# Kernel optimization log

Measured on AMD Instinct MI355X. Metric: run time of the kernel, lower is better.

Reference implementation:

```python
import jax, jax.numpy as jnp
import numpy as np

N_NODES = 20000
N_EDGES = 160000
N_GRAPHS = 64
DIMS = [9, 128, 256, 512, 1534]
NEG_SLOPE_ATT = 0.2   # GATConv attention LeakyReLU
NEG_SLOPE_ACT = 0.01  # nn.LeakyReLU between layers
EPS = 1e-5            # GraphNorm eps


def setup_inputs() -> dict:
    key = jax.random.key(0)
    inp = {}
    k, key = jax.random.split(key)
    inp['x'] = jax.random.normal(k, (N_NODES, DIMS[0]), jnp.float32)
    k, key = jax.random.split(key)
    inp['edge_index'] = jax.random.randint(k, (2, N_EDGES), 0, N_NODES)
    k, key = jax.random.split(key)
    inp['batch'] = jnp.sort(jax.random.randint(k, (N_NODES,), 0, N_GRAPHS))
    for l in range(4):
        din, dout = DIMS[l], DIMS[l + 1]
        k1, k2, k3, key = jax.random.split(key, 4)
        s = 1.0 / np.sqrt(din)
        inp[f'W{l}'] = (jax.random.normal(k1, (din, dout)) * s).astype(jnp.float32)
        inp[f'asrc{l}'] = (jax.random.normal(k2, (dout,)) * 0.1).astype(jnp.float32)
        inp[f'adst{l}'] = (jax.random.normal(k3, (dout,)) * 0.1).astype(jnp.float32)
        inp[f'b{l}'] = jnp.zeros((dout,), jnp.float32)
        inp[f'g{l}'] = jnp.ones((dout,), jnp.float32)   # GraphNorm weight
        inp[f'bt{l}'] = jnp.zeros((dout,), jnp.float32)  # GraphNorm bias
        inp[f'ms{l}'] = jnp.ones((dout,), jnp.float32)   # GraphNorm mean_scale
    return inp


def _gat_conv(h, src, dst, n, W, asrc, adst, b):
    # PyG GATConv, heads=1: linear (no bias), edge attention, segment softmax, scatter-add
    hp = h @ W                                                    # [N, dout]
    e = jax.nn.leaky_relu((hp @ asrc)[src] + (hp @ adst)[dst], NEG_SLOPE_ATT)  # [E]
    m = jax.ops.segment_max(e, dst, num_segments=n)
    m = jnp.where(jnp.isfinite(m), m, 0.0)
    ex = jnp.exp(e - m[dst])
    denom = jax.ops.segment_sum(ex, dst, num_segments=n)
    alpha = ex / (denom[dst] + 1e-16)                             # [E]
    out = jax.ops.segment_sum(alpha[:, None] * hp[src], dst, num_segments=n)
    return out + b


def _graph_norm(h, batch, counts, g, bt, ms):
    # PyG GraphNorm: per-graph mean/var with learnable mean_scale
    mean = jax.ops.segment_sum(h, batch, num_segments=N_GRAPHS) / counts
    out = h - ms * mean[batch]
    var = jax.ops.segment_sum(out * out, batch, num_segments=N_GRAPHS) / counts
    return out / jnp.sqrt(var[batch] + EPS) * g + bt


def _forward(x, edge_index, batch, params):
    n = x.shape[0]
    loops = jnp.arange(n)
    src = jnp.concatenate([edge_index[0], loops])   # GATConv add_self_loops=True
    dst = jnp.concatenate([edge_index[1], loops])
    counts = jax.ops.segment_sum(jnp.ones((n,), x.dtype), batch, num_segments=N_GRAPHS)[:, None]
    h = x
    for (W, asrc, adst, b, g, bt, ms) in params:
        h = _gat_conv(h, src, dst, n, W, asrc, adst, b)
        h = jax.nn.leaky_relu(h, NEG_SLOPE_ACT)
        h = _graph_norm(h, batch, counts, g, bt, ms)
        # Dropout(p=0.1) is identity in eval mode
    mean = (jax.ops.segment_sum(h, batch, num_segments=N_GRAPHS) / counts)[:, None, :]
    mx = jax.ops.segment_max(h, batch, num_segments=N_GRAPHS)[:, None, :]
    return jnp.concatenate([mean, mx], axis=1)      # [G, 2, 1534]


def reference(x, edge_index, batch,
              W0, asrc0, adst0, b0, g0, bt0, ms0,
              W1, asrc1, adst1, b1, g1, bt1, ms1,
              W2, asrc2, adst2, b2, g2, bt2, ms2,
              W3, asrc3, adst3, b3, g3, bt3, ms3):
    params = [
        (W0, asrc0, adst0, b0, g0, bt0, ms0),
        (W1, asrc1, adst1, b1, g1, bt1, ms1),
        (W2, asrc2, adst2, b2, g2, bt2, ms2),
        (W3, asrc3, adst3, b3, g3, bt3, ms3),
    ]
    return _forward(x, edge_index, batch, params)
```

## Files before the change

### kernel.cpp

```cpp
#include <hip/hip_runtime.h>
#include <math.h>

typedef unsigned int u32;
typedef unsigned short u16;
using half8 = __attribute__((ext_vector_type(8))) _Float16;
using f32x4 = __attribute__((ext_vector_type(4))) float;

#define NN 20000
#define MPAD 20096
#define NE 160000
#define ET 180000
#define NG 64
#define NBLK 79

constexpr float NEG_ATT = 0.2f;
constexpr float NEG_ACT = 0.01f;
constexpr float EPS_GN  = 1e-5f;

struct Ptr4 { const float *p0, *p1, *p2, *p3; };


__device__ __forceinline__ u16 f2h(float f) {
    _Float16 h = (_Float16)f;
    return __builtin_bit_cast(u16, h);
}
__device__ __forceinline__ float h2f(u16 b) {
    return (float)__builtin_bit_cast(_Float16, b);
}

__device__ __forceinline__ void gl_lds16(const void* g, void* l) {
    __builtin_amdgcn_global_load_lds((const __attribute__((address_space(1))) u32*)g,
                                     (__attribute__((address_space(3))) u32*)l, 16, 0, 0);
}

__device__ __forceinline__ float lrelu_att(float v) {
    return (v > 0.f) ? v : NEG_ATT * v;
}


__global__ void k_bounds(const int* __restrict__ batch, int* __restrict__ counts,
                         int* __restrict__ gstart) {
    __shared__ int ls[NG + 1];
    int g = threadIdx.x;
    int lo = 0, hi = NN;
    while (lo < hi) {
        int mid = (lo + hi) >> 1;
        if (batch[mid] < g) lo = mid + 1; else hi = mid;
    }
    ls[g] = lo;
    if (g == 0) ls[NG] = NN;
    __syncthreads();
    counts[g] = ls[g + 1] - ls[g];
    gstart[g] = ls[g];
    if (g == 0) gstart[NG] = NN;
}


__global__ void k_deg(const int* __restrict__ ei, int* deg) {
    int i = blockIdx.x * 256 + threadIdx.x;
    if (i >= ET) return;
    int dst = (i < NE) ? ei[NE + i] : (i - NE);
    atomicAdd(&deg[dst], 1);
}

__global__ void k_scan1(const int* __restrict__ deg, int* __restrict__ bsum) {
    int i = blockIdx.x * 256 + threadIdx.x;
    int v = (i < NN) ? deg[i] : 0;
    int lane = threadIdx.x & 63, w = threadIdx.x >> 6;
    #pragma unroll
    for (int off = 32; off; off >>= 1) v += __shfl_down(v, off, 64);
    __shared__ int ws[4];
    if (lane == 0) ws[w] = v;
    __syncthreads();
    if (threadIdx.x == 0) bsum[blockIdx.x] = ws[0] + ws[1] + ws[2] + ws[3];
}

__global__ void k_scan2(const int* __restrict__ bsum, int* __restrict__ boff,
                        int* __restrict__ total) {
    int tid = threadIdx.x;
    int v = (tid < NBLK) ? bsum[tid] : 0;
    int lane = tid & 63, w = tid >> 6;
    int val = v;
    #pragma unroll
    for (int off = 1; off < 64; off <<= 1) {
        int t = __shfl_up(val, off, 64);
        if (lane >= off) val += t;
    }
    __shared__ int ws[4];
    if (lane == 63) ws[w] = val;
    __syncthreads();
    int woff = 0;
    for (int k = 0; k < w; k++) woff += ws[k];
    int excl = woff + val - v;
    if (tid < NBLK) boff[tid] = excl;
    if (tid == NBLK - 1) *total = excl + v;
}

__global__ void k_scan3(const int* __restrict__ deg, const int* __restrict__ boff,
                        int* __restrict__ row_ptr, int* __restrict__ cursor) {
    int i = blockIdx.x * 256 + threadIdx.x;
    int v = (i < NN) ? deg[i] : 0;
    int lane = threadIdx.x & 63, w = threadIdx.x >> 6;
    int val = v;
    #pragma unroll
    for (int off = 1; off < 64; off <<= 1) {
        int t = __shfl_up(val, off, 64);
        if (lane >= off) val += t;
    }
    __shared__ int ws[4];
    if (lane == 63) ws[w] = val;
    __syncthreads();
    int woff = 0;
    for (int k = 0; k < w; k++) woff += ws[k];
    int excl = boff[blockIdx.x] + woff + val - v;
    if (i < NN) { row_ptr[i] = excl; cursor[i] = excl; }
}

__global__ void k_scatter(const int* __restrict__ ei, int* cursor, int* __restrict__ col) {
    int i = blockIdx.x * 256 + threadIdx.x;
    if (i >= ET) return;
    int s, d;
    if (i < NE) { s = ei[i]; d = ei[NE + i]; } else { s = i - NE; d = s; }
    int p = atomicAdd(&cursor[d], 1);
    col[p] = s;
}


__global__ void k_wvec_all(Ptr4 W, Ptr4 As, Ptr4 Ad,
                           float* __restrict__ wsrcA, float* __restrict__ wdstA) {
    const int dins[4]  = {9, 128, 256, 512};
    const int douts[4] = {128, 256, 512, 1534};
    int l = blockIdx.y, k = blockIdx.x;
    if (k >= dins[l]) return;
    const float* Wp = (l == 0) ? W.p0 : (l == 1) ? W.p1 : (l == 2) ? W.p2 : W.p3;
    const float* as = (l == 0) ? As.p0 : (l == 1) ? As.p1 : (l == 2) ? As.p2 : As.p3;
    const float* ad = (l == 0) ? Ad.p0 : (l == 1) ? Ad.p1 : (l == 2) ? Ad.p2 : Ad.p3;
    int NC = douts[l];
    const float* row = Wp + (size_t)k * NC;
    float ss = 0.f, sd = 0.f;
    for (int n = threadIdx.x; n < NC; n += 256) {
        float w = row[n];
        ss += w * as[n];
        sd += w * ad[n];
    }
    __shared__ float ls[8];
    int lane = threadIdx.x & 63, w4 = threadIdx.x >> 6;
    #pragma unroll
    for (int off = 32; off; off >>= 1) {
        ss += __shfl_down(ss, off, 64);
        sd += __shfl_down(sd, off, 64);
    }
    if (lane == 0) { ls[w4] = ss; ls[4 + w4] = sd; }
    __syncthreads();
    if (threadIdx.x == 0) {
        wsrcA[l * 512 + k] = ls[0] + ls[1] + ls[2] + ls[3];
        wdstA[l * 512 + k] = ls[4] + ls[5] + ls[6] + ls[7];
    }
}


__global__ void k_wbt_all(Ptr4 W, u16* __restrict__ WbTall) {
    const int Ks[3] = {128, 256, 512};
    const int NCs[3] = {256, 512, 1534};
    const int Nps[3] = {256, 512, 1536};
    const size_t offs[3] = {0, 256 * 128, 256 * 128 + 512 * 256};
    int l = blockIdx.z;
    int K = Ks[l], NC = NCs[l], Np = Nps[l];
    int n0 = blockIdx.x * 32, k0 = blockIdx.y * 32;
    if (n0 >= Np || k0 >= K) return;
    const float* Wp = (l == 0) ? W.p1 : (l == 1) ? W.p2 : W.p3;
    u16* WbT = WbTall + offs[l];
    __shared__ u16 tile[32][33];
    int tx = threadIdx.x & 31, ty = threadIdx.x >> 5;
    #pragma unroll
    for (int i = 0; i < 4; i++) {
        int k = k0 + ty + i * 8, n = n0 + tx;
        float v = (k < K && n < NC) ? Wp[(size_t)k * NC + n] : 0.f;
        tile[ty + i * 8][tx] = f2h(v);
    }
    __syncthreads();
    #pragma unroll
    for (int i = 0; i < 4; i++) {
        int n = n0 + ty + i * 8, k = k0 + tx;
        if (n < Np && k < K) WbT[(size_t)n * K + k] = tile[tx][ty + i * 8];
    }
}


__global__ void k_scores0(const float* __restrict__ x, const float* __restrict__ wsrc,
                          const float* __restrict__ wdst, float* __restrict__ s_src,
                          float* __restrict__ s_dst) {
    int v = blockIdx.x * 256 + threadIdx.x;
    if (v >= NN) return;
    const float* r = x + (size_t)v * 9;
    float ss = 0.f, sd = 0.f;
    #pragma unroll
    for (int k = 0; k < 9; k++) { ss += r[k] * wsrc[k]; sd += r[k] * wdst[k]; }
    s_src[v] = ss; s_dst[v] = sd;
}

template <int VW>
__global__ void k_scores_h(const u16* __restrict__ h, const float* __restrict__ wsrc,
                           const float* __restrict__ wdst, float* __restrict__ s_src,
                           float* __restrict__ s_dst, int din) {
    int v = blockIdx.x * 4 + (threadIdx.x >> 6);
    int lane = threadIdx.x & 63;
    if (v >= NN) return;
    const u16* row = h + (size_t)v * din;
    float ss = 0.f, sd = 0.f;
    for (int d = lane * VW; d < din; d += 64 * VW) {
        u32 ua[VW / 2];
        if constexpr (VW == 2) {
            ua[0] = *(const u32*)(row + d);
        } else if constexpr (VW == 4) {
            uint2 t = *(const uint2*)(row + d);
            ua[0] = t.x; ua[1] = t.y;
        } else {
            uint4 t = *(const uint4*)(row + d);
            ua[0] = t.x; ua[1] = t.y; ua[2] = t.z; ua[3] = t.w;
        }
        #pragma unroll
        for (int j = 0; j < VW / 2; j++) {
            float h0 = h2f((u16)(ua[j] & 0xffffu)), h1 = h2f((u16)(ua[j] >> 16));
            ss += h0 * wsrc[d + 2 * j] + h1 * wsrc[d + 2 * j + 1];
            sd += h0 * wdst[d + 2 * j] + h1 * wdst[d + 2 * j + 1];
        }
    }
    #pragma unroll
    for (int off = 32; off; off >>= 1) {
        ss += __shfl_down(ss, off, 64);
        sd += __shfl_down(sd, off, 64);
    }
    if (lane == 0) { s_src[v] = ss; s_dst[v] = sd; }
}


template <int TPN, int CPT>
__global__ __launch_bounds__(256) void k_agg_fused(const u16* __restrict__ h,
                                                   const int* __restrict__ row_ptr,
                                                   const int* __restrict__ col,
                                                   const float* __restrict__ s_src,
                                                   const float* __restrict__ s_dst,
                                                   u16* __restrict__ agg, int din) {
    constexpr int NPB = 256 / TPN;
    __shared__ float sm[NPB * 2];
    int grp = threadIdx.x / TPN;
    int lane = threadIdx.x % TPN;
    int v = blockIdx.x * NPB + grp;
    bool valid = v < NN;
    int st = 0, en = 0;
    float sd = 0.f;
    if (valid) { st = row_ptr[v]; en = row_ptr[v + 1]; sd = s_dst[v]; }

    float mx = -INFINITY;
    if (valid && lane < 64) {
        for (int p = st + lane; p < en; p += 64)
            mx = fmaxf(mx, lrelu_att(s_src[col[p]] + sd));
    }
    #pragma unroll
    for (int off = 32; off; off >>= 1) mx = fmaxf(mx, __shfl_xor(mx, off, 64));
    float sum = 0.f;
    if (valid && lane < 64) {
        for (int p = st + lane; p < en; p += 64)
            sum += __expf(lrelu_att(s_src[col[p]] + sd) - mx);
    }
    #pragma unroll
    for (int off = 32; off; off >>= 1) sum += __shfl_xor(sum, off, 64);
    if (lane == 0) { sm[grp * 2] = mx; sm[grp * 2 + 1] = 1.0f / (sum + 1e-16f); }
    __syncthreads();
    if (!valid) return;
    float m = sm[grp * 2], inv = sm[grp * 2 + 1];

    int d0 = lane * 2 * CPT;
    float acc[2 * CPT];
    #pragma unroll
    for (int i = 0; i < 2 * CPT; i++) acc[i] = 0.f;
    const u16* hb = h + d0;
    int p = st;
    for (; p + 2 <= en; p += 2) {
        int c0 = col[p], c1 = col[p + 1];
        float a0 = __expf(lrelu_att(s_src[c0] + sd) - m);
        float a1 = __expf(lrelu_att(s_src[c1] + sd) - m);
        u32 u0[CPT], u1[CPT];
        if constexpr (CPT == 1) {
            u0[0] = *(const u32*)(hb + (size_t)c0 * din);
            u1[0] = *(const u32*)(hb + (size_t)c1 * din);
        } else {
            uint2 t0 = *(const uint2*)(hb + (size_t)c0 * din);
            uint2 t1 = *(const uint2*)(hb + (size_t)c1 * din);
            u0[0] = t0.x; u0[1] = t0.y; u1[0] = t1.x; u1[1] = t1.y;
        }
        #pragma unroll
        for (int wv = 0; wv < CPT; wv++) {
            acc[2 * wv]     += a0 * h2f((u16)(u0[wv] & 0xffffu)) + a1 * h2f((u16)(u1[wv] & 0xffffu));
            acc[2 * wv + 1] += a0 * h2f((u16)(u0[wv] >> 16))     + a1 * h2f((u16)(u1[wv] >> 16));
        }
    }
    if (p < en) {
        int c0 = col[p];
        float a0 = __expf(lrelu_att(s_src[c0] + sd) - m);
        u32 u0[CPT];
        if constexpr (CPT == 1) {
            u0[0] = *(const u32*)(hb + (size_t)c0 * din);
        } else {
            uint2 t0 = *(const uint2*)(hb + (size_t)c0 * din);
            u0[0] = t0.x; u0[1] = t0.y;
        }
        #pragma unroll
        for (int wv = 0; wv < CPT; wv++) {
            acc[2 * wv]     += a0 * h2f((u16)(u0[wv] & 0xffffu));
            acc[2 * wv + 1] += a0 * h2f((u16)(u0[wv] >> 16));
        }
    }
    u32 o[CPT];
    #pragma unroll
    for (int wv = 0; wv < CPT; wv++)
        o[wv] = (u32)f2h(acc[2 * wv] * inv) | ((u32)f2h(acc[2 * wv + 1] * inv) << 16);
    if constexpr (CPT == 1) {
        *(u32*)(agg + (size_t)v * din + d0) = o[0];
    } else {
        uint2 ov; ov.x = o[0]; ov.y = o[1];
        *(uint2*)(agg + (size_t)v * din + d0) = ov;
    }
}

__global__ __launch_bounds__(256) void k_agg0_fused(const float* __restrict__ x,
                                                    const int* __restrict__ row_ptr,
                                                    const int* __restrict__ col,
                                                    const float* __restrict__ s_src,
                                                    const float* __restrict__ s_dst,
                                                    float* __restrict__ agg0) {
    __shared__ float sm[4 * 2];
    int grp = threadIdx.x >> 6;
    int lane = threadIdx.x & 63;
    int v = blockIdx.x * 4 + grp;
    bool valid = v < NN;
    int st = 0, en = 0;
    float sd = 0.f;
    if (valid) { st = row_ptr[v]; en = row_ptr[v + 1]; sd = s_dst[v]; }
    float mx = -INFINITY;
    if (valid) {
        for (int p = st + lane; p < en; p += 64)
            mx = fmaxf(mx, lrelu_att(s_src[col[p]] + sd));
    }
    #pragma unroll
    for (int off = 32; off; off >>= 1) mx = fmaxf(mx, __shfl_xor(mx, off, 64));
    float sum = 0.f;
    if (valid) {
        for (int p = st + lane; p < en; p += 64)
            sum += __expf(lrelu_att(s_src[col[p]] + sd) - mx);
    }
    #pragma unroll
    for (int off = 32; off; off >>= 1) sum += __shfl_xor(sum, off, 64);
    if (lane == 0) { sm[grp * 2] = mx; sm[grp * 2 + 1] = 1.0f / (sum + 1e-16f); }
    __syncthreads();
    if (!valid || lane >= 9) return;
    float m = sm[grp * 2], inv = sm[grp * 2 + 1];
    float acc = 0.f;
    for (int p = st; p < en; p++) {
        int c = col[p];
        float a = __expf(lrelu_att(s_src[c] + sd) - m);
        acc += a * x[(size_t)c * 9 + lane];
    }
    agg0[(size_t)v * 9 + lane] = acc * inv;
}


__global__ __launch_bounds__(256) void k_gemm0(const float* __restrict__ agg0,
                                               const float* __restrict__ W,
                                               const float* __restrict__ bias,
                                               u16* __restrict__ out) {
    __shared__ float Ws[9 * 128];
    for (int i = threadIdx.x; i < 9 * 128; i += 256) Ws[i] = W[i];
    __syncthreads();
    int node = blockIdx.x * 2 + (threadIdx.x >> 7);
    int n = threadIdx.x & 127;
    if (node >= NN) return;
    const float* xr = agg0 + (size_t)node * 9;
    float acc = bias[n];
    #pragma unroll
    for (int k = 0; k < 9; k++) acc += xr[k] * Ws[k * 128 + n];
    acc = (acc > 0.f) ? acc : NEG_ACT * acc;
    out[(size_t)node * 128 + n] = f2h(acc);
}


#define BM 128
#define BK 32

__global__ __launch_bounds__(256) void k_gemm_f16(const u16* __restrict__ A,
                                                  const u16* __restrict__ B,
                                                  const float* __restrict__ bias,
                                                  u16* __restrict__ C,
                                                  int K, int ldC, int NC, int ntx) {
    int nwg = gridDim.x;
    int b = blockIdx.x;
    int q = nwg >> 3, r = nwg & 7;
    int xcd = b & 7, idx = b >> 3;
    int wg = (xcd < r ? xcd * (q + 1) : r * (q + 1) + (xcd - r) * q) + idx;
    int row0 = (wg / ntx) * BM;
    int col0 = (wg % ntx) * BM;

    __shared__ u16 lds[2][2][BM * BK];
    int tid = threadIdx.x;
    int lane = tid & 63, w = tid >> 6;
    int wr = w >> 1, wc = w & 1;

    f32x4 acc[4][4];
    #pragma unroll
    for (int m = 0; m < 4; m++)
        #pragma unroll
        for (int n = 0; n < 4; n++)
            #pragma unroll
            for (int rr2 = 0; rr2 < 4; rr2++) acc[m][n][rr2] = 0.f;

    int nt = K / BK;

    auto stage = [&](int buf, int t) {
        int k0 = t * BK;
        #pragma unroll
        for (int c = 0; c < 2; c++) {
            int idx2 = tid + c * 256;
            int rr2 = idx2 >> 2, kc = idx2 & 3;
            int kcs = kc ^ (rr2 & 3);
            gl_lds16(A + (size_t)(row0 + rr2) * K + k0 + kcs * 8, &lds[buf][0][idx2 * 8]);
            gl_lds16(B + (size_t)(col0 + rr2) * K + k0 + kcs * 8, &lds[buf][1][idx2 * 8]);
        }
    };

    auto compute = [&](int buf) {
        const u16* As = &lds[buf][0][0];
        const u16* Bs = &lds[buf][1][0];
        int kg = lane >> 4, rl = lane & 15;
        half8 af[4], bfr[4];
        #pragma unroll
        for (int m = 0; m < 4; m++) {
            int rr2 = wr * 64 + m * 16 + rl;
            af[m] = *(const half8*)(As + rr2 * BK + (kg ^ (rr2 & 3)) * 8);
        }
        #pragma unroll
        for (int n = 0; n < 4; n++) {
            int rr2 = wc * 64 + n * 16 + rl;
            bfr[n] = *(const half8*)(Bs + rr2 * BK + (kg ^ (rr2 & 3)) * 8);
        }
        #pragma unroll
        for (int m = 0; m < 4; m++)
            #pragma unroll
            for (int n = 0; n < 4; n++)
                acc[m][n] = __builtin_amdgcn_mfma_f32_16x16x32_f16(af[m], bfr[n], acc[m][n], 0, 0, 0);
    };

    stage(0, 0);
    __syncthreads();
    for (int t = 0; t < nt; t++) {
        if (t + 1 < nt) stage((t + 1) & 1, t + 1);
        compute(t & 1);
        __syncthreads();
    }

    u16* ep = ((u16*)lds) + w * (32 * 72);
    int kg = lane >> 4, rl = lane & 15;
    int rrow = lane >> 3;
    int c8 = (lane & 7) * 8;
    #pragma unroll
    for (int half = 0; half < 2; half++) {
        #pragma unroll
        for (int m2 = 0; m2 < 2; m2++) {
            int m = half * 2 + m2;
            #pragma unroll
            for (int n = 0; n < 4; n++) {
                int colg = col0 + wc * 64 + n * 16 + rl;
                float bb = (colg < NC) ? bias[colg] : 0.f;
                #pragma unroll
                for (int rr2 = 0; rr2 < 4; rr2++) {
                    float o = acc[m][n][rr2] + bb;
                    o = (o > 0.f) ? o : NEG_ACT * o;
                    ep[(m2 * 16 + kg * 4 + rr2) * 72 + n * 16 + rl] = f2h(o);
                }
            }
        }
        #pragma unroll
        for (int it = 0; it < 4; it++) {
            int rloc = it * 8 + rrow;
            half8 vv = *(const half8*)(ep + rloc * 72 + c8);
            int rowg = row0 + wr * 64 + half * 32 + rloc;
            *(half8*)(C + (size_t)rowg * ldC + col0 + wc * 64 + c8) = vv;
        }
    }
}


__global__ __launch_bounds__(1024, 4) void k_gemm256(const u16* __restrict__ A,
                                                     const u16* __restrict__ B,
                                                     const float* __restrict__ bias,
                                                     u16* __restrict__ C,
                                                     int K, int ldC, int NC, int ntx, int M) {
    __shared__ u16 sMem[65536];
    #define SA(buf, h) (sMem + (buf) * 16384 + (h) * 8192)
    #define SB(buf, h) (sMem + 32768 + (buf) * 16384 + (h) * 8192)

    int nwg = gridDim.x, b = blockIdx.x;
    int q = nwg >> 3, r = nwg & 7;
    int xcd = b & 7, bidx = b >> 3;
    int wg = (xcd < r ? xcd * (q + 1) : r * (q + 1) + (xcd - r) * q) + bidx;
    int row0 = (wg / ntx) * 256;
    int col0 = (wg % ntx) * 256;

    int tid = threadIdx.x;
    int w = tid >> 6, lane = tid & 63;
    int wm = w >> 2, wn = w & 3;
    int rl = lane & 15, kg = lane >> 4;
    int ksl = (kg ^ ((rl >> 1) & 3)) * 8;

    f32x4 acc[4][4];
    #pragma unroll
    for (int m = 0; m < 4; m++)
        #pragma unroll
        for (int n = 0; n < 4; n++)
            #pragma unroll
            for (int i = 0; i < 4; i++) acc[m][n][i] = 0.f;

    {
        int rr = tid >> 2, s = tid & 3;
        int ss = s ^ ((rr >> 1) & 3);
        int ra = row0 + rr; ra = (ra < M) ? ra : (M - 1);
        const u16* aSrc0 = A + (size_t)ra * K + ss * 8;
        const u16* bSrc0 = B + (size_t)(col0 + rr) * K + ss * 8;
        u16* ldsDst = sMem + tid * 8;

        auto stageA = [&](int h, int t, int buf) {
            gl_lds16(aSrc0 + t * 64 + h * 32, ldsDst + buf * 16384 + h * 8192);
        };
        auto stageB = [&](int h, int t, int buf) {
            gl_lds16(bSrc0 + t * 64 + h * 32, ldsDst + 32768 + buf * 16384 + h * 8192);
        };

        half8 af[4], bf0, bf1;
        auto ldA4 = [&](int buf, int h) {
            #pragma unroll
            for (int i = 0; i < 4; i++)
                af[i] = *(const half8*)(SA(buf, h) + (wm * 64 + i * 16 + rl) * 32 + ksl);
        };
        auto ldB2 = [&](int buf, int h, int n0) {
            bf0 = *(const half8*)(SB(buf, h) + (wn * 64 + n0 * 16 + rl) * 32 + ksl);
            bf1 = *(const half8*)(SB(buf, h) + (wn * 64 + (n0 + 1) * 16 + rl) * 32 + ksl);
        };
        auto mm8 = [&](int n0) {
            __builtin_amdgcn_s_setprio(1);
            #pragma unroll
            for (int i = 0; i < 4; i++) {
                acc[i][n0]     = __builtin_amdgcn_mfma_f32_16x16x32_f16(af[i], bf0, acc[i][n0], 0, 0, 0);
                acc[i][n0 + 1] = __builtin_amdgcn_mfma_f32_16x16x32_f16(af[i], bf1, acc[i][n0 + 1], 0, 0, 0);
            }
            __builtin_amdgcn_s_setprio(0);
        };

        #define PH_PRE() do { __builtin_amdgcn_sched_barrier(0); \
                              __builtin_amdgcn_s_barrier(); \
                              asm volatile("s_waitcnt lgkmcnt(0)" ::: "memory"); \
                              __builtin_amdgcn_sched_barrier(0); } while (0)
        #define PH_POST() do { __builtin_amdgcn_sched_barrier(0); \
                               __builtin_amdgcn_s_barrier(); \
                               __builtin_amdgcn_sched_barrier(0); } while (0)

        int nt = K >> 6;

        stageA(0, 0, 0); stageB(0, 0, 0); stageA(1, 0, 0); stageB(1, 0, 0);
        asm volatile("s_waitcnt vmcnt(2)" ::: "memory");
        PH_POST();

        for (int t = 0; t < nt; t++) {
            int rb = t & 1, wb = rb ^ 1;
            bool pf = (t + 1 < nt);
            ldA4(rb, 0); ldB2(rb, 0, 0);
            if (pf) stageA(0, t + 1, wb);
            PH_PRE();
            mm8(0);
            PH_POST();
            ldB2(rb, 0, 2);
            if (pf) stageB(0, t + 1, wb);
            PH_PRE();
            mm8(2);
            __builtin_amdgcn_sched_barrier(0);
            if (pf) asm volatile("s_waitcnt vmcnt(2)" ::: "memory");
            else    asm volatile("s_waitcnt vmcnt(0)" ::: "memory");
            PH_POST();
            ldA4(rb, 1); ldB2(rb, 1, 0);
            if (pf) stageA(1, t + 1, wb);
            PH_PRE();
            mm8(0);
            PH_POST();
            ldB2(rb, 1, 2);
            if (pf) stageB(1, t + 1, wb);
            PH_PRE();
            mm8(2);
            __builtin_amdgcn_sched_barrier(0);
            if (pf) asm volatile("s_waitcnt vmcnt(2)" ::: "memory");
            PH_POST();
        }
        #undef PH_PRE
        #undef PH_POST
    }

    u16* ep = sMem + w * (32 * 72);
    float bv[4];
    #pragma unroll
    for (int n = 0; n < 4; n++) {
        int colg = col0 + wn * 64 + n * 16 + rl;
        bv[n] = (colg < NC) ? bias[colg] : 0.f;
    }
    int rrow = lane >> 3, c8 = (lane & 7) * 8;
    #pragma unroll
    for (int mh = 0; mh < 2; mh++) {
        #pragma unroll
        for (int msub = 0; msub < 2; msub++) {
            int m = mh * 2 + msub;
            #pragma unroll
            for (int n = 0; n < 4; n++) {
                #pragma unroll
                for (int rg = 0; rg < 4; rg++) {
                    float o = acc[m][n][rg] + bv[n];
                    o = (o > 0.f) ? o : NEG_ACT * o;
                    ep[(msub * 16 + kg * 4 + rg) * 72 + n * 16 + rl] = f2h(o);
                }
            }
        }
        #pragma unroll
        for (int it = 0; it < 4; it++) {
            int rloc = it * 8 + rrow;
            half8 vv = *(const half8*)(ep + rloc * 72 + c8);
            int rowg = row0 + wm * 64 + mh * 32 + rloc;
            if (rowg < M)
                *(half8*)(C + (size_t)rowg * ldC + col0 + wn * 64 + c8) = vv;
        }
    }
    #undef SA
    #undef SB
}


__global__ __launch_bounds__(256) void k_gn_stats2(const u16* __restrict__ h,
                                                   const int* __restrict__ gstart,
                                                   float* __restrict__ gsum,
                                                   float* __restrict__ gsq, int ld) {
    int g = blockIdx.x;
    int c0 = blockIdx.y * 128;
    int ct = threadIdx.x & 15, rg = threadIdx.x >> 4;
    int d0 = c0 + ct * 8;
    int st = gstart[g], en = gstart[g + 1];
    float s[8], qq[8];
    #pragma unroll
    for (int i = 0; i < 8; i++) { s[i] = 0.f; qq[i] = 0.f; }
    for (int r = st + rg; r < en; r += 16) {
        uint4 u = *(const uint4*)(h + (size_t)r * ld + d0);
        u32 ua[4] = {u.x, u.y, u.z, u.w};
        #pragma unroll
        for (int j = 0; j < 4; j++) {
            float v0 = h2f((u16)(ua[j] & 0xffffu)), v1 = h2f((u16)(ua[j] >> 16));
            s[2 * j] += v0; s[2 * j + 1] += v1;
            qq[2 * j] += v0 * v0; qq[2 * j + 1] += v1 * v1;
        }
    }
    __shared__ float Ls[16][128], Lq[16][128];
    #pragma unroll
    for (int i = 0; i < 8; i++) { Ls[rg][ct * 8 + i] = s[i]; Lq[rg][ct * 8 + i] = qq[i]; }
    __syncthreads();
    int tid = threadIdx.x;
    if (tid < 128) {
        float ss = 0.f, sq = 0.f;
        #pragma unroll
        for (int r2 = 0; r2 < 16; r2++) { ss += Ls[r2][tid]; sq += Lq[r2][tid]; }
        gsum[(size_t)g * ld + c0 + tid] = ss;
        gsq[(size_t)g * ld + c0 + tid] = sq;
    }
}

template <int CT>
__global__ __launch_bounds__(256) void k_gn_apply_n(const u16* __restrict__ h,
                           const int* __restrict__ batch,
                           const float* __restrict__ gsum, const float* __restrict__ gsq,
                           const int* __restrict__ counts, const float* __restrict__ ms,
                           const float* __restrict__ gam, const float* __restrict__ bet,
                           u16* __restrict__ out, int ld) {
    constexpr int RPB = (256 / CT) * 4;
    int ct = threadIdx.x % CT, rg = threadIdx.x / CT;
    int d0 = ct * 8;
    int r0 = blockIdx.x * RPB + rg * 4;
    float msv[8], gv[8], bv[8];
    #pragma unroll
    for (int i = 0; i < 8; i++) { msv[i] = ms[d0 + i]; gv[i] = gam[d0 + i]; bv[i] = bet[d0 + i]; }
    int gcur = -1;
    float sub[8], sc[8];
    #pragma unroll
    for (int i = 0; i < 8; i++) { sub[i] = 0.f; sc[i] = 0.f; }
    #pragma unroll
    for (int rr = 0; rr < 4; rr++) {
        int r = r0 + rr;
        if (r < NN) {
            int g = batch[r];
            if (g != gcur) {
                gcur = g;
                float inv = 1.0f / (float)counts[g];
                #pragma unroll
                for (int i = 0; i < 8; i++) {
                    float mean = gsum[(size_t)g * ld + d0 + i] * inv;
                    float q2   = gsq[(size_t)g * ld + d0 + i] * inv;
                    float var  = fmaxf(q2 - (2.f * msv[i] - msv[i] * msv[i]) * mean * mean, 0.f);
                    sub[i] = msv[i] * mean;
                    sc[i]  = gv[i] * rsqrtf(var + EPS_GN);
                }
            }
            uint4 u = *(const uint4*)(h + (size_t)r * ld + d0);
            u32 ua[4] = {u.x, u.y, u.z, u.w};
            uint4 wv4;
            u32 wo[4];
            #pragma unroll
            for (int j = 0; j < 4; j++) {
                float o0 = (h2f((u16)(ua[j] & 0xffffu)) - sub[2 * j]) * sc[2 * j] + bv[2 * j];
                float o1 = (h2f((u16)(ua[j] >> 16)) - sub[2 * j + 1]) * sc[2 * j + 1] + bv[2 * j + 1];
                wo[j] = (u32)f2h(o0) | ((u32)f2h(o1) << 16);
            }
            wv4.x = wo[0]; wv4.y = wo[1]; wv4.z = wo[2]; wv4.w = wo[3];
            *(uint4*)(out + (size_t)r * ld + d0) = wv4;
        }
    }
}

__global__ __launch_bounds__(256) void k_gn_pool(const u16* __restrict__ h,
                           const int* __restrict__ gstart,
                           const float* __restrict__ gsum, const float* __restrict__ gsq,
                           const float* __restrict__ ms, const float* __restrict__ gam,
                           const float* __restrict__ bet, float* __restrict__ out,
                           int dout, int ld) {
    int g = blockIdx.x;
    int c0 = blockIdx.y * 128;
    int ct = threadIdx.x & 15, rg = threadIdx.x >> 4;
    int d0 = c0 + ct * 8;
    int st = gstart[g], en = gstart[g + 1];
    float inv = 1.0f / (float)(en - st);
    float sub[8], sc[8], bv[8];
    #pragma unroll
    for (int i = 0; i < 8; i++) {
        int d = d0 + i;
        int dc = (d < dout) ? d : (dout - 1);
        float msv = ms[dc];
        float mean = gsum[(size_t)g * ld + d] * inv;
        float q2   = gsq[(size_t)g * ld + d] * inv;
        float var  = fmaxf(q2 - (2.f * msv - msv * msv) * mean * mean, 0.f);
        sub[i] = msv * mean;
        sc[i]  = gam[dc] * rsqrtf(var + EPS_GN);
        bv[i]  = bet[dc];
    }
    float s[8], mx[8];
    #pragma unroll
    for (int i = 0; i < 8; i++) { s[i] = 0.f; mx[i] = -INFINITY; }
    for (int r = st + rg; r < en; r += 16) {
        uint4 u = *(const uint4*)(h + (size_t)r * ld + d0);
        u32 ua[4] = {u.x, u.y, u.z, u.w};
        #pragma unroll
        for (int j = 0; j < 4; j++) {
            float o0 = (h2f((u16)(ua[j] & 0xffffu)) - sub[2 * j]) * sc[2 * j] + bv[2 * j];
            float o1 = (h2f((u16)(ua[j] >> 16)) - sub[2 * j + 1]) * sc[2 * j + 1] + bv[2 * j + 1];
            s[2 * j] += o0; s[2 * j + 1] += o1;
            mx[2 * j] = fmaxf(mx[2 * j], o0); mx[2 * j + 1] = fmaxf(mx[2 * j + 1], o1);
        }
    }
    __shared__ float Ls[16][128], Lm[16][128];
    #pragma unroll
    for (int i = 0; i < 8; i++) { Ls[rg][ct * 8 + i] = s[i]; Lm[rg][ct * 8 + i] = mx[i]; }
    __syncthreads();
    int tid = threadIdx.x;
    if (tid < 128) {
        float ss = 0.f, mm = -INFINITY;
        #pragma unroll
        for (int r2 = 0; r2 < 16; r2++) { ss += Ls[r2][tid]; mm = fmaxf(mm, Lm[r2][tid]); }
        int d = c0 + tid;
        if (d < dout) {
            out[(size_t)g * 2 * dout + d] = ss * inv;
            out[(size_t)g * 2 * dout + dout + d] = mm;
        }
    }
}


extern "C" void kernel_launch(void* const* d_in, const int* in_sizes, int n_in,
                              void* d_out, int out_size, void* d_ws, size_t ws_size,
                              hipStream_t stream) {
    const float* x = (const float*)d_in[0];
    const int* ei = (const int*)d_in[1];
    const int* batch = (const int*)d_in[2];
    const float *Wl[4], *Asr[4], *Ads[4], *Bi[4], *Ga[4], *Be[4], *Ms[4];
    for (int l = 0; l < 4; l++) {
        int b = 3 + 7 * l;
        Wl[l]  = (const float*)d_in[b];
        Asr[l] = (const float*)d_in[b + 1];
        Ads[l] = (const float*)d_in[b + 2];
        Bi[l]  = (const float*)d_in[b + 3];
        Ga[l]  = (const float*)d_in[b + 4];
        Be[l]  = (const float*)d_in[b + 5];
        Ms[l]  = (const float*)d_in[b + 6];
    }

    char* ws = (char*)d_ws;
    size_t off = 0;
    auto alloc = [&](size_t bytes) -> char* {
        char* p = ws + off;
        off += (bytes + 255) & ~(size_t)255;
        return p;
    };
    u16*   actA   = (u16*)alloc((size_t)MPAD * 512 * 2);
    u16*   actB   = (u16*)alloc((size_t)MPAD * 1536 * 2);
    u16*   agg    = (u16*)alloc((size_t)MPAD * 512 * 2);
    float* agg0   = (float*)alloc((size_t)NN * 9 * 4);
    u16*   WbTall = (u16*)alloc((size_t)(256 * 128 + 512 * 256 + 1536 * 512) * 2);
    float* wsrcA  = (float*)alloc((size_t)4 * 512 * 4);
    float* wdstA  = (float*)alloc((size_t)4 * 512 * 4);
    float* s_src  = (float*)alloc((size_t)NN * 4);
    float* s_dst  = (float*)alloc((size_t)NN * 4);
    int* row_ptr  = (int*)alloc((size_t)(NN + 1) * 4);
    int* cursor   = (int*)alloc((size_t)NN * 4);
    int* colA     = (int*)alloc((size_t)ET * 4);
    int* counts   = (int*)alloc((size_t)NG * 4);
    int* gstart   = (int*)alloc((size_t)(NG + 1) * 4);
    int* bsum     = (int*)alloc((size_t)NBLK * 4);
    int* boff     = (int*)alloc((size_t)NBLK * 4);
    float* gsumA  = (float*)alloc((size_t)4 * NG * 1536 * 4);
    float* gsqA   = (float*)alloc((size_t)4 * NG * 1536 * 4);

    char* zbase = ws + off;
    int* deg      = (int*)alloc((size_t)NN * 4);
    size_t zbytes = (size_t)((ws + off) - zbase);
    hipMemsetAsync(zbase, 0, zbytes, stream);

    k_bounds<<<1, 64, 0, stream>>>(batch, counts, gstart);
    k_deg<<<(ET + 255) / 256, 256, 0, stream>>>(ei, deg);
    k_scan1<<<NBLK, 256, 0, stream>>>(deg, bsum);
    k_scan2<<<1, 256, 0, stream>>>(bsum, boff, row_ptr + NN);
    k_scan3<<<NBLK, 256, 0, stream>>>(deg, boff, row_ptr, cursor);
    k_scatter<<<(ET + 255) / 256, 256, 0, stream>>>(ei, cursor, colA);

    Ptr4 Wp{Wl[0], Wl[1], Wl[2], Wl[3]};
    Ptr4 Ap{Asr[0], Asr[1], Asr[2], Asr[3]};
    Ptr4 Dp{Ads[0], Ads[1], Ads[2], Ads[3]};
    k_wvec_all<<<dim3(512, 4), 256, 0, stream>>>(Wp, Ap, Dp, wsrcA, wdstA);
    k_wbt_all<<<dim3(48, 16, 3), 256, 0, stream>>>(Wp, WbTall);

    const int dims[5] = {9, 128, 256, 512, 1534};
    const size_t wbtOffs[3] = {0, 256 * 128, 256 * 128 + 512 * 256};
    const int RT256 = (MPAD + 255) / 256;

    for (int l = 0; l < 4; l++) {
        int din = dims[l], dout = dims[l + 1];
        int ldo = (dout == 1534) ? 1536 : dout;
        float* gsum = gsumA + (size_t)l * NG * 1536;
        float* gsq  = gsqA  + (size_t)l * NG * 1536;
        const float* wsrc = wsrcA + l * 512;
        const float* wdst = wdstA + l * 512;

        if (l == 0) {
            k_scores0<<<(NN + 255) / 256, 256, 0, stream>>>(x, wsrc, wdst, s_src, s_dst);
            k_agg0_fused<<<(NN + 3) / 4, 256, 0, stream>>>(x, row_ptr, colA, s_src, s_dst, agg0);
            k_gemm0<<<(NN + 1) / 2, 256, 0, stream>>>(agg0, Wl[0], Bi[0], actB);
        } else if (l == 1) {
            k_scores_h<2><<<(NN + 3) / 4, 256, 0, stream>>>(actA, wsrc, wdst, s_src, s_dst, din);
            k_agg_fused<64, 1><<<(NN + 3) / 4, 256, 0, stream>>>(actA, row_ptr, colA, s_src, s_dst, agg, din);
            int ntx = ldo / 128;
            int nwg = ntx * (MPAD / 128);
            k_gemm_f16<<<nwg, 256, 0, stream>>>(agg, WbTall + wbtOffs[0], Bi[1], actB,
                                                din, ldo, dout, ntx);
        } else {
            if (din == 256) {
                k_scores_h<4><<<(NN + 3) / 4, 256, 0, stream>>>(actA, wsrc, wdst, s_src, s_dst, din);
                k_agg_fused<64, 2><<<(NN + 3) / 4, 256, 0, stream>>>(actA, row_ptr, colA, s_src, s_dst, agg, din);
            } else {
                k_scores_h<8><<<(NN + 3) / 4, 256, 0, stream>>>(actA, wsrc, wdst, s_src, s_dst, din);
                k_agg_fused<128, 2><<<(NN + 1) / 2, 256, 0, stream>>>(actA, row_ptr, colA, s_src, s_dst, agg, din);
            }
            int ntx = ldo / 256;
            int nwg = ntx * RT256;
            k_gemm256<<<nwg, 1024, 0, stream>>>(agg, WbTall + wbtOffs[l - 1], Bi[l], actB,
                                                din, ldo, dout, ntx, MPAD);
        }

        k_gn_stats2<<<dim3(NG, ldo / 128), 256, 0, stream>>>(actB, gstart, gsum, gsq, ldo);
        if (l == 0)
            k_gn_apply_n<16><<<(NN + 63) / 64, 256, 0, stream>>>(actB, batch, gsum, gsq, counts,
                                                                 Ms[0], Ga[0], Be[0], actA, 128);
        else if (l == 1)
            k_gn_apply_n<32><<<(NN + 31) / 32, 256, 0, stream>>>(actB, batch, gsum, gsq, counts,
                                                                 Ms[1], Ga[1], Be[1], actA, 256);
        else if (l == 2)
            k_gn_apply_n<64><<<(NN + 15) / 16, 256, 0, stream>>>(actB, batch, gsum, gsq, counts,
                                                                 Ms[2], Ga[2], Be[2], actA, 512);
        else
            k_gn_pool<<<dim3(NG, 12), 256, 0, stream>>>(actB, gstart, gsum, gsq,
                                                        Ms[3], Ga[3], Be[3], (float*)d_out,
                                                        1534, 1536);
    }
}
```

Before: 336.8 us.

## Triple-buffer GEMM K=32 pipeline and fuse GraphNorm stats with apply/pool

The 256x256 GEMM drops its double-buffered K=64 stage with four barrier phases. In its place is a 3-stage ring of K=32 tiles with a single barrier per step, prefetching two tiles ahead. Separately, the GraphNorm statistics kernel is merged with the apply kernel and with the final pooling kernel, so per-graph sums stay in shared memory and one launch plus the global stats buffers disappear. The cost is that each fused block now reads its rows twice and only 64*ncol blocks do the apply work, so parallelism is lower than the old row-parallel apply.

```diff
diff --git a/kernel.cpp b/kernel.cpp
--- a/kernel.cpp
+++ b/kernel.cpp
@@ -495,9 +495,7 @@
                                                      const float* __restrict__ bias,
                                                      u16* __restrict__ C,
                                                      int K, int ldC, int NC, int ntx, int M) {
-    __shared__ u16 sMem[65536];
-    #define SA(buf, h) (sMem + (buf) * 16384 + (h) * 8192)
-    #define SB(buf, h) (sMem + 32768 + (buf) * 16384 + (h) * 8192)
+    __shared__ u16 sMem[49152];
 
     int nwg = gridDim.x, b = blockIdx.x;
     int q = nwg >> 3, r = nwg & 7;
@@ -526,80 +524,53 @@
         int ra = row0 + rr; ra = (ra < M) ? ra : (M - 1);
         const u16* aSrc0 = A + (size_t)ra * K + ss * 8;
         const u16* bSrc0 = B + (size_t)(col0 + rr) * K + ss * 8;
-        u16* ldsDst = sMem + tid * 8;
-
-        auto stageA = [&](int h, int t, int buf) {
-            gl_lds16(aSrc0 + t * 64 + h * 32, ldsDst + buf * 16384 + h * 8192);
+        u16* dstA = sMem + tid * 8;
+        u16* dstB = sMem + 8192 + tid * 8;
+
+        auto stage = [&](int t, int bf2) {
+            gl_lds16(aSrc0 + t * 32, dstA + bf2 * 16384);
+            gl_lds16(bSrc0 + t * 32, dstB + bf2 * 16384);
         };
-        auto stageB = [&](int h, int t, int buf) {
-            gl_lds16(bSrc0 + t * 64 + h * 32, ldsDst + 32768 + buf * 16384 + h * 8192);
-        };
-
-        half8 af[4], bf0, bf1;
-        auto ldA4 = [&](int buf, int h) {
+
+        half8 af[4], bf[4];
+        auto ldAB = [&](int bf2) {
+            const u16* Ab = sMem + bf2 * 16384;
+            const u16* Bb = Ab + 8192;
             #pragma unroll
             for (int i = 0; i < 4; i++)
-                af[i] = *(const half8*)(SA(buf, h) + (wm * 64 + i * 16 + rl) * 32 + ksl);
+                af[i] = *(const half8*)(Ab + (wm * 64 + i * 16 + rl) * 32 + ksl);
+            #pragma unroll
+            for (int i = 0; i < 4; i++)
+                bf[i] = *(const half8*)(Bb + (wn * 64 + i * 16 + rl) * 32 + ksl);
         };
-        auto ldB2 = [&](int buf, int h, int n0) {
-            bf0 = *(const half8*)(SB(buf, h) + (wn * 64 + n0 * 16 + rl) * 32 + ksl);
-            bf1 = *(const half8*)(SB(buf, h) + (wn * 64 + (n0 + 1) * 16 + rl) * 32 + ksl);
-        };
-        auto mm8 = [&](int n0) {
+
+        int nt = K >> 5;
+
+        stage(0, 0); stage(1, 1);
+        __builtin_amdgcn_sched_barrier(0);
+        asm volatile("s_waitcnt vmcnt(2)" ::: "memory");
+        __builtin_amdgcn_s_barrier();
+        __builtin_amdgcn_sched_barrier(0);
+
+        int rb = 0;
+        for (int t = 0; t < nt; t++) {
+            int sb = rb + 2; if (sb >= 3) sb -= 3;
+            if (t + 2 < nt) stage(t + 2, sb);
+            ldAB(rb);
             __builtin_amdgcn_s_setprio(1);
             #pragma unroll
-            for (int i = 0; i < 4; i++) {
-                acc[i][n0]     = __builtin_amdgcn_mfma_f32_16x16x32_f16(af[i], bf0, acc[i][n0], 0, 0, 0);
-                acc[i][n0 + 1] = __builtin_amdgcn_mfma_f32_16x16x32_f16(af[i], bf1, acc[i][n0 + 1], 0, 0, 0);
-            }
+            for (int i = 0; i < 4; i++)
+                #pragma unroll
+                for (int n = 0; n < 4; n++)
+                    acc[i][n] = __builtin_amdgcn_mfma_f32_16x16x32_f16(af[i], bf[n], acc[i][n], 0, 0, 0);
             __builtin_amdgcn_s_setprio(0);
-        };
-
-        #define PH_PRE() do { __builtin_amdgcn_sched_barrier(0); \
-                              __builtin_amdgcn_s_barrier(); \
-                              asm volatile("s_waitcnt lgkmcnt(0)" ::: "memory"); \
-                              __builtin_amdgcn_sched_barrier(0); } while (0)
-        #define PH_POST() do { __builtin_amdgcn_sched_barrier(0); \
-                               __builtin_amdgcn_s_barrier(); \
-                               __builtin_amdgcn_sched_barrier(0); } while (0)
-
-        int nt = K >> 6;
-
-        stageA(0, 0, 0); stageB(0, 0, 0); stageA(1, 0, 0); stageB(1, 0, 0);
-        asm volatile("s_waitcnt vmcnt(2)" ::: "memory");
-        PH_POST();
-
-        for (int t = 0; t < nt; t++) {
-            int rb = t & 1, wb = rb ^ 1;
-            bool pf = (t + 1 < nt);
-            ldA4(rb, 0); ldB2(rb, 0, 0);
-            if (pf) stageA(0, t + 1, wb);
-            PH_PRE();
-            mm8(0);
-            PH_POST();
-            ldB2(rb, 0, 2);
-            if (pf) stageB(0, t + 1, wb);
-            PH_PRE();
-            mm8(2);
             __builtin_amdgcn_sched_barrier(0);
-            if (pf) asm volatile("s_waitcnt vmcnt(2)" ::: "memory");
-            else    asm volatile("s_waitcnt vmcnt(0)" ::: "memory");
-            PH_POST();
-            ldA4(rb, 1); ldB2(rb, 1, 0);
-            if (pf) stageA(1, t + 1, wb);
-            PH_PRE();
-            mm8(0);
-            PH_POST();
-            ldB2(rb, 1, 2);
-            if (pf) stageB(1, t + 1, wb);
-            PH_PRE();
-            mm8(2);
+            if (t + 2 < nt)      asm volatile("s_waitcnt vmcnt(2)" ::: "memory");
+            else if (t + 1 < nt) asm volatile("s_waitcnt vmcnt(0)" ::: "memory");
+            __builtin_amdgcn_s_barrier();
             __builtin_amdgcn_sched_barrier(0);
-            if (pf) asm volatile("s_waitcnt vmcnt(2)" ::: "memory");
-            PH_POST();
-        }
-        #undef PH_PRE
-        #undef PH_POST
+            rb = (rb == 2) ? 0 : rb + 1;
+        }
     }
 
     u16* ep = sMem + w * (32 * 72);
@@ -634,20 +605,19 @@
                 *(half8*)(C + (size_t)rowg * ldC + col0 + wn * 64 + c8) = vv;
         }
     }
-    #undef SA
-    #undef SB
-}
-
-
-__global__ __launch_bounds__(256) void k_gn_stats2(const u16* __restrict__ h,
-                                                   const int* __restrict__ gstart,
-                                                   float* __restrict__ gsum,
-                                                   float* __restrict__ gsq, int ld) {
+}
+
+
+__global__ __launch_bounds__(256) void k_gn_fused(const u16* __restrict__ h,
+                           const int* __restrict__ gstart,
+                           const float* __restrict__ ms, const float* __restrict__ gam,
+                           const float* __restrict__ bet, u16* __restrict__ out, int ld) {
     int g = blockIdx.x;
     int c0 = blockIdx.y * 128;
     int ct = threadIdx.x & 15, rg = threadIdx.x >> 4;
     int d0 = c0 + ct * 8;
     int st = gstart[g], en = gstart[g + 1];
+    float inv = 1.0f / (float)(en - st);
     float s[8], qq[8];
     #pragma unroll
     for (int i = 0; i < 8; i++) { s[i] = 0.f; qq[i] = 0.f; }
@@ -669,66 +639,40 @@
     if (tid < 128) {
         float ss = 0.f, sq = 0.f;
         #pragma unroll
-        for (int r2 = 0; r2 < 16; r2++) { ss += Ls[r2][tid]; sq += Lq[r2][tid]; }
-        gsum[(size_t)g * ld + c0 + tid] = ss;
-        gsq[(size_t)g * ld + c0 + tid] = sq;
-    }
-}
-
-template <int CT>
-__global__ __launch_bounds__(256) void k_gn_apply_n(const u16* __restrict__ h,
-                           const int* __restrict__ batch,
-                           const float* __restrict__ gsum, const float* __restrict__ gsq,
-                           const int* __restrict__ counts, const float* __restrict__ ms,
-                           const float* __restrict__ gam, const float* __restrict__ bet,
-                           u16* __restrict__ out, int ld) {
-    constexpr int RPB = (256 / CT) * 4;
-    int ct = threadIdx.x % CT, rg = threadIdx.x / CT;
-    int d0 = ct * 8;
-    int r0 = blockIdx.x * RPB + rg * 4;
-    float msv[8], gv[8], bv[8];
-    #pragma unroll
-    for (int i = 0; i < 8; i++) { msv[i] = ms[d0 + i]; gv[i] = gam[d0 + i]; bv[i] = bet[d0 + i]; }
-    int gcur = -1;
-    float sub[8], sc[8];
-    #pragma unroll
-    for (int i = 0; i < 8; i++) { sub[i] = 0.f; sc[i] = 0.f; }
-    #pragma unroll
-    for (int rr = 0; rr < 4; rr++) {
-        int r = r0 + rr;
-        if (r < NN) {
-            int g = batch[r];
-            if (g != gcur) {
-                gcur = g;
-                float inv = 1.0f / (float)counts[g];
-                #pragma unroll
-                for (int i = 0; i < 8; i++) {
-                    float mean = gsum[(size_t)g * ld + d0 + i] * inv;
-                    float q2   = gsq[(size_t)g * ld + d0 + i] * inv;
-                    float var  = fmaxf(q2 - (2.f * msv[i] - msv[i] * msv[i]) * mean * mean, 0.f);
-                    sub[i] = msv[i] * mean;
-                    sc[i]  = gv[i] * rsqrtf(var + EPS_GN);
-                }
-            }
-            uint4 u = *(const uint4*)(h + (size_t)r * ld + d0);
-            u32 ua[4] = {u.x, u.y, u.z, u.w};
-            uint4 wv4;
-            u32 wo[4];
-            #pragma unroll
-            for (int j = 0; j < 4; j++) {
-                float o0 = (h2f((u16)(ua[j] & 0xffffu)) - sub[2 * j]) * sc[2 * j] + bv[2 * j];
-                float o1 = (h2f((u16)(ua[j] >> 16)) - sub[2 * j + 1]) * sc[2 * j + 1] + bv[2 * j + 1];
-                wo[j] = (u32)f2h(o0) | ((u32)f2h(o1) << 16);
-            }
-            wv4.x = wo[0]; wv4.y = wo[1]; wv4.z = wo[2]; wv4.w = wo[3];
-            *(uint4*)(out + (size_t)r * ld + d0) = wv4;
-        }
-    }
-}
-
-__global__ __launch_bounds__(256) void k_gn_pool(const u16* __restrict__ h,
+        for (int r2 = 1; r2 < 16; r2++) { ss += Ls[r2][tid]; sq += Lq[r2][tid]; }
+        Ls[0][tid] += ss; Lq[0][tid] += sq;
+    }
+    __syncthreads();
+    float sub[8], sc[8], bv[8];
+    #pragma unroll
+    for (int i = 0; i < 8; i++) {
+        int cl = ct * 8 + i, d = d0 + i;
+        float msv = ms[d];
+        float mean = Ls[0][cl] * inv;
+        float q2   = Lq[0][cl] * inv;
+        float var  = fmaxf(q2 - (2.f * msv - msv * msv) * mean * mean, 0.f);
+        sub[i] = msv * mean;
+        sc[i]  = gam[d] * rsqrtf(var + EPS_GN);
+        bv[i]  = bet[d];
+    }
+    for (int r = st + rg; r < en; r += 16) {
+        uint4 u = *(const uint4*)(h + (size_t)r * ld + d0);
+        u32 ua[4] = {u.x, u.y, u.z, u.w};
+        uint4 wv4;
+        u32 wo[4];
+        #pragma unroll
+        for (int j = 0; j < 4; j++) {
+            float o0 = (h2f((u16)(ua[j] & 0xffffu)) - sub[2 * j]) * sc[2 * j] + bv[2 * j];
+            float o1 = (h2f((u16)(ua[j] >> 16)) - sub[2 * j + 1]) * sc[2 * j + 1] + bv[2 * j + 1];
+            wo[j] = (u32)f2h(o0) | ((u32)f2h(o1) << 16);
+        }
+        wv4.x = wo[0]; wv4.y = wo[1]; wv4.z = wo[2]; wv4.w = wo[3];
+        *(uint4*)(out + (size_t)r * ld + d0) = wv4;
+    }
+}
+
+__global__ __launch_bounds__(256) void k_gn_poolf(const u16* __restrict__ h,
                            const int* __restrict__ gstart,
-                           const float* __restrict__ gsum, const float* __restrict__ gsq,
                            const float* __restrict__ ms, const float* __restrict__ gam,
                            const float* __restrict__ bet, float* __restrict__ out,
                            int dout, int ld) {
@@ -738,22 +682,47 @@
     int d0 = c0 + ct * 8;
     int st = gstart[g], en = gstart[g + 1];
     float inv = 1.0f / (float)(en - st);
+    float s[8], qq[8];
+    #pragma unroll
+    for (int i = 0; i < 8; i++) { s[i] = 0.f; qq[i] = 0.f; }
+    for (int r = st + rg; r < en; r += 16) {
+        uint4 u = *(const uint4*)(h + (size_t)r * ld + d0);
+        u32 ua[4] = {u.x, u.y, u.z, u.w};
+        #pragma unroll
+        for (int j = 0; j < 4; j++) {
+            float v0 = h2f((u16)(ua[j] & 0xffffu)), v1 = h2f((u16)(ua[j] >> 16));
+            s[2 * j] += v0; s[2 * j + 1] += v1;
+            qq[2 * j] += v0 * v0; qq[2 * j + 1] += v1 * v1;
+        }
+    }
+    __shared__ float Ls[16][128], Lq[16][128];
+    #pragma unroll
+    for (int i = 0; i < 8; i++) { Ls[rg][ct * 8 + i] = s[i]; Lq[rg][ct * 8 + i] = qq[i]; }
+    __syncthreads();
+    int tid = threadIdx.x;
+    if (tid < 128) {
+        float ss = 0.f, sq = 0.f;
+        #pragma unroll
+        for (int r2 = 1; r2 < 16; r2++) { ss += Ls[r2][tid]; sq += Lq[r2][tid]; }
+        Ls[0][tid] += ss; Lq[0][tid] += sq;
+    }
+    __syncthreads();
     float sub[8], sc[8], bv[8];
     #pragma unroll
     for (int i = 0; i < 8; i++) {
-        int d = d0 + i;
+        int cl = ct * 8 + i, d = d0 + i;
         int dc = (d < dout) ? d : (dout - 1);
         float msv = ms[dc];
-        float mean = gsum[(size_t)g * ld + d] * inv;
-        float q2   = gsq[(size_t)g * ld + d] * inv;
+        float mean = Ls[0][cl] * inv;
+        float q2   = Lq[0][cl] * inv;
         float var  = fmaxf(q2 - (2.f * msv - msv * msv) * mean * mean, 0.f);
         sub[i] = msv * mean;
         sc[i]  = gam[dc] * rsqrtf(var + EPS_GN);
         bv[i]  = bet[dc];
     }
-    float s[8], mx[8];
-    #pragma unroll
-    for (int i = 0; i < 8; i++) { s[i] = 0.f; mx[i] = -INFINITY; }
+    float ps[8], pm[8];
+    #pragma unroll
+    for (int i = 0; i < 8; i++) { ps[i] = 0.f; pm[i] = -INFINITY; }
     for (int r = st + rg; r < en; r += 16) {
         uint4 u = *(const uint4*)(h + (size_t)r * ld + d0);
         u32 ua[4] = {u.x, u.y, u.z, u.w};
@@ -761,19 +730,18 @@
         for (int j = 0; j < 4; j++) {
             float o0 = (h2f((u16)(ua[j] & 0xffffu)) - sub[2 * j]) * sc[2 * j] + bv[2 * j];
             float o1 = (h2f((u16)(ua[j] >> 16)) - sub[2 * j + 1]) * sc[2 * j + 1] + bv[2 * j + 1];
-            s[2 * j] += o0; s[2 * j + 1] += o1;
-            mx[2 * j] = fmaxf(mx[2 * j], o0); mx[2 * j + 1] = fmaxf(mx[2 * j + 1], o1);
-        }
-    }
-    __shared__ float Ls[16][128], Lm[16][128];
-    #pragma unroll
-    for (int i = 0; i < 8; i++) { Ls[rg][ct * 8 + i] = s[i]; Lm[rg][ct * 8 + i] = mx[i]; }
-    __syncthreads();
-    int tid = threadIdx.x;
+            ps[2 * j] += o0; ps[2 * j + 1] += o1;
+            pm[2 * j] = fmaxf(pm[2 * j], o0); pm[2 * j + 1] = fmaxf(pm[2 * j + 1], o1);
+        }
+    }
+    __syncthreads();
+    #pragma unroll
+    for (int i = 0; i < 8; i++) { Ls[rg][ct * 8 + i] = ps[i]; Lq[rg][ct * 8 + i] = pm[i]; }
+    __syncthreads();
     if (tid < 128) {
         float ss = 0.f, mm = -INFINITY;
         #pragma unroll
-        for (int r2 = 0; r2 < 16; r2++) { ss += Ls[r2][tid]; mm = fmaxf(mm, Lm[r2][tid]); }
+        for (int r2 = 0; r2 < 16; r2++) { ss += Ls[r2][tid]; mm = fmaxf(mm, Lq[r2][tid]); }
         int d = c0 + tid;
         if (d < dout) {
             out[(size_t)g * 2 * dout + d] = ss * inv;
@@ -824,8 +792,6 @@
     int* gstart   = (int*)alloc((size_t)(NG + 1) * 4);
     int* bsum     = (int*)alloc((size_t)NBLK * 4);
     int* boff     = (int*)alloc((size_t)NBLK * 4);
-    float* gsumA  = (float*)alloc((size_t)4 * NG * 1536 * 4);
-    float* gsqA   = (float*)alloc((size_t)4 * NG * 1536 * 4);
 
     char* zbase = ws + off;
     int* deg      = (int*)alloc((size_t)NN * 4);
@@ -852,8 +818,6 @@
     for (int l = 0; l < 4; l++) {
         int din = dims[l], dout = dims[l + 1];
         int ldo = (dout == 1534) ? 1536 : dout;
-        float* gsum = gsumA + (size_t)l * NG * 1536;
-        float* gsq  = gsqA  + (size_t)l * NG * 1536;
         const float* wsrc = wsrcA + l * 512;
         const float* wdst = wdstA + l * 512;
 
@@ -882,19 +846,12 @@
                                                 din, ldo, dout, ntx, MPAD);
         }
 
-        k_gn_stats2<<<dim3(NG, ldo / 128), 256, 0, stream>>>(actB, gstart, gsum, gsq, ldo);
-        if (l == 0)
-            k_gn_apply_n<16><<<(NN + 63) / 64, 256, 0, stream>>>(actB, batch, gsum, gsq, counts,
-                                                                 Ms[0], Ga[0], Be[0], actA, 128);
-        else if (l == 1)
-            k_gn_apply_n<32><<<(NN + 31) / 32, 256, 0, stream>>>(actB, batch, gsum, gsq, counts,
-                                                                 Ms[1], Ga[1], Be[1], actA, 256);
-        else if (l == 2)
-            k_gn_apply_n<64><<<(NN + 15) / 16, 256, 0, stream>>>(actB, batch, gsum, gsq, counts,
-                                                                 Ms[2], Ga[2], Be[2], actA, 512);
+        if (l < 3)
+            k_gn_fused<<<dim3(NG, ldo / 128), 256, 0, stream>>>(actB, gstart,
+                                                                Ms[l], Ga[l], Be[l], actA, ldo);
         else
-            k_gn_pool<<<dim3(NG, 12), 256, 0, stream>>>(actB, gstart, gsum, gsq,
-                                                        Ms[3], Ga[3], Be[3], (float*)d_out,
-                                                        1534, 1536);
-    }
-}
+            k_gn_poolf<<<dim3(NG, 12), 256, 0, stream>>>(actB, gstart,
+                                                         Ms[3], Ga[3], Be[3], (float*)d_out,
+                                                         1534, 1536);
+    }
+}
```

After: 332.9 us. No clear change (-1.2%).
